# Kernel tuning notes

Measured on AMD Instinct MI355X. Metric: run time of the kernel, lower is better.

The kernel has to match this reference:

```python
import jax, jax.numpy as jnp
import numpy as np

S = 2        # subsample_rate
EPS = 1e-5   # BatchNorm eps


def maxpool(x, k):
    B, C, H, W = x.shape
    return x.reshape(B, C, H // k, k, W // k, k).max(axis=(3, 5))


def conv1x1(x, w, b):
    # x: [B,C,H,W], w: [O,C], b: [O]
    return jnp.einsum('bchw,oc->bohw', x, w) + b[None, :, None, None]


def upsample_bilinear_ac(y, s):
    # torch nn.Upsample(mode='bilinear', scale_factor=s, align_corners=True)
    B, C, h, w = y.shape
    H, W = h * s, w * s
    ri = jnp.arange(H, dtype=jnp.float32) * ((h - 1) / (H - 1))
    ci = jnp.arange(W, dtype=jnp.float32) * ((w - 1) / (W - 1))
    r0 = jnp.floor(ri).astype(jnp.int32); r1 = jnp.minimum(r0 + 1, h - 1)
    c0 = jnp.floor(ci).astype(jnp.int32); c1 = jnp.minimum(c0 + 1, w - 1)
    wr = (ri - r0)[None, None, :, None]
    wc = (ci - c0)[None, None, None, :]
    top = y[:, :, r0, :] * (1.0 - wr) + y[:, :, r1, :] * wr
    return top[:, :, :, c0] * (1.0 - wc) + top[:, :, :, c1] * wc


def setup_inputs() -> dict:
    key = jax.random.key(0)
    ks = jax.random.split(key, 12)
    B, C, IC, H, W = 4, 256, 128, 192, 192
    sc = 0.05  # keep attention logits in a sane range
    x = jax.random.normal(ks[0], (B, C, H, W), jnp.float32)
    g_w = jax.random.normal(ks[1], (IC, C), jnp.float32) * sc
    g_b = jax.random.normal(ks[2], (IC,), jnp.float32) * sc
    theta_w = jax.random.normal(ks[3], (IC, C), jnp.float32) * sc
    theta_b = jax.random.normal(ks[4], (IC,), jnp.float32) * sc
    phi_w = jax.random.normal(ks[5], (IC, C), jnp.float32) * sc
    phi_b = jax.random.normal(ks[6], (IC,), jnp.float32) * sc
    W_w = jax.random.normal(ks[7], (C, IC, 3, 3), jnp.float32) * sc
    W_b = jax.random.normal(ks[8], (C,), jnp.float32) * sc
    bn_gamma = jnp.ones((C,), jnp.float32)
    bn_beta = jnp.zeros((C,), jnp.float32)
    bn_mean = jax.random.normal(ks[9], (C,), jnp.float32) * sc
    bn_var = jax.random.uniform(ks[10], (C,), jnp.float32) + 0.5
    return dict(x=x, g_w=g_w, g_b=g_b, theta_w=theta_w, theta_b=theta_b,
                phi_w=phi_w, phi_b=phi_b, W_w=W_w, W_b=W_b,
                bn_gamma=bn_gamma, bn_beta=bn_beta, bn_mean=bn_mean, bn_var=bn_var)


def reference(x, g_w, g_b, theta_w, theta_b, phi_w, phi_b, W_w, W_b,
              bn_gamma, bn_beta, bn_mean, bn_var):
    B, C, H, Wd = x.shape
    IC = g_w.shape[0]
    xp = maxpool(x, S)                               # [B,C,H/S,W/S]
    theta = conv1x1(xp, theta_w, theta_b)            # [B,IC,h,w]
    g = maxpool(conv1x1(xp, g_w, g_b), 2)            # [B,IC,h/2,w/2]
    phi = maxpool(conv1x1(xp, phi_w, phi_b), 2)      # [B,IC,h/2,w/2]
    h, w = theta.shape[2], theta.shape[3]
    th = theta.reshape(B, IC, h * w).transpose(0, 2, 1)   # [B,Nt,IC]
    ph = phi.reshape(B, IC, -1)                           # [B,IC,Np]
    gx = g.reshape(B, IC, -1).transpose(0, 2, 1)          # [B,Np,IC]
    f = jnp.einsum('bnc,bcm->bnm', th, ph)                # [B,Nt,Np]
    a = jax.nn.softmax(f, axis=-1)
    y = jnp.einsum('bnm,bmc->bnc', a, gx)                 # [B,Nt,IC]
    y = y.transpose(0, 2, 1).reshape(B, IC, h, w)
    y = upsample_bilinear_ac(y, S)                        # [B,IC,H,W]
    wy = jax.lax.conv_general_dilated(
        y, W_w, (1, 1), ((1, 1), (1, 1)),
        dimension_numbers=('NCHW', 'OIHW', 'NCHW')) + W_b[None, :, None, None]
    inv = bn_gamma / jnp.sqrt(bn_var + EPS)
    wy = (wy - bn_mean[None, :, None, None]) * inv[None, :, None, None] + bn_beta[None, :, None, None]
    return (wy + x, wy)
```

## Files before the change

kernel.cpp:

```cpp
#include <hip/hip_runtime.h>
#include <hip/hip_bf16.h>
#include <math.h>

#define B_   4
#define C_   256
#define ICH  128
#define H_   192
#define W_   192
#define hs   96
#define ws2  96
#define HW   (hs*ws2)
#define HP   48
#define WP   48
#define NP   (HP*WP)
#define EPSB 1e-5f
#define PADW 194
#define TOT  ((size_t)B_*C_*H_*W_)

#define QB 128
#define KB 64
#define NT (NP/KB)
#define SM_OFF 20.0f

using bf16x8 = __attribute__((ext_vector_type(8))) short;
using f32x4  = __attribute__((ext_vector_type(4))) float;
using f32x16 = __attribute__((ext_vector_type(16))) float;

#define OFF_XPB   ((size_t)0)
#define OFF_THB   ((size_t)4718592)
#define OFF_PHB   ((size_t)7077888)
#define OFF_GVT   ((size_t)7667712)
#define OFF_WB3   ((size_t)8257536)
#define OFF_Y96N  ((size_t)8306688)
#define OFF_ST    ((size_t)13025280)
#define OFF_WT    ((size_t)13025792)
#define OFF_YPAD  ((size_t)13173248)

static __device__ __forceinline__ float b2f(unsigned short u) {
  union { unsigned int i; float f; } c; c.i = (unsigned int)u << 16; return c.f;
}

__global__ __launch_bounds__(256) void k_pool2(const float* __restrict__ x,
                                               __hip_bfloat16* __restrict__ xpb) {
  __shared__ float lds[96 * 33];
  int t  = threadIdx.x;
  int pi = blockIdx.x;
  int cg = blockIdx.y;
  int b  = blockIdx.z;
  const float* xb = x + (((size_t)b * C_ + cg * 32) * H_ + 2 * pi) * W_;
#pragma unroll
  for (int rr = 0; rr < 6; ++rr) {
    int e = rr * 256 + t;
    int c  = e / 48;
    int cq = e % 48;
    const float* src = xb + (size_t)c * H_ * W_ + cq * 4;
    float4 A = *(const float4*)src;
    float4 Bv = *(const float4*)(src + W_);
    float pe = fmaxf(fmaxf(A.x, A.y), fmaxf(Bv.x, Bv.y));
    float po = fmaxf(fmaxf(A.z, A.w), fmaxf(Bv.z, Bv.w));
    lds[(2 * cq) * 33 + c]     = pe;
    lds[(2 * cq + 1) * 33 + c] = po;
  }
  __syncthreads();
  __hip_bfloat16* ob = xpb + ((size_t)b * HW + pi * ws2) * C_ + cg * 32;
#pragma unroll
  for (int rr = 0; rr < 2; ++rr) {
    int w = rr * 256 + t;
    if (w < 384) {
      int pj = w >> 2, oc = w & 3;
      union { ushort u[8]; uint4 v; } pk;
#pragma unroll
      for (int k = 0; k < 8; ++k) {
        __hip_bfloat16 hv = __float2bfloat16(lds[pj * 33 + oc * 8 + k]);
        pk.u[k] = *(ushort*)&hv;
      }
      *(uint4*)(ob + (size_t)pj * C_ + oc * 8) = pk.v;
    }
  }
}

__global__ __launch_bounds__(256) void k_prep(const float* __restrict__ Ww,
                                              const float* __restrict__ tw,
                                              const float* __restrict__ gw,
                                              const float* __restrict__ pw,
                                              const float* __restrict__ Wb,
                                              const float* __restrict__ bg,
                                              const float* __restrict__ bb,
                                              const float* __restrict__ bm,
                                              const float* __restrict__ bv,
                                              __hip_bfloat16* __restrict__ Wt,
                                              __hip_bfloat16* __restrict__ wb3,
                                              float* __restrict__ ST) {
  int bid = blockIdx.x;
  int t = threadIdx.x;
  if (bid < 1152) {
    int idx = bid * 256 + t;
    int lo  = idx & 7;
    int o   = (idx >> 3) & 255;
    int ic8 = (idx >> 11) & 15;
    int tap = idx >> 15;
    int ic  = ic8 * 8 + lo;
    Wt[idx] = __float2bfloat16(Ww[(size_t)o * (ICH * 9) + ic * 9 + tap]);
  } else if (bid < 1536) {
    int idx = (bid - 1152) * 256 + t;
    int set = idx >> 15; int rem = idx & 32767;
    const float* src = set == 0 ? tw : (set == 1 ? gw : pw);
    wb3[idx] = __float2bfloat16(src[rem]);
  } else {
    float sc = bg[t] * rsqrtf(bv[t] + EPSB);
    ST[t] = sc;
    ST[256 + t] = (Wb[t] - bm[t]) * sc + bb[t];
  }
}

__global__ __launch_bounds__(256) void k_qkv2(
    const __hip_bfloat16* __restrict__ xpb,
    const __hip_bfloat16* __restrict__ wb3,
    const float* __restrict__ tb, const float* __restrict__ gb_,
    const float* __restrict__ pb_,
    __hip_bfloat16* __restrict__ thb,
    __hip_bfloat16* __restrict__ gvt,
    __hip_bfloat16* __restrict__ phb) {
  __shared__ __align__(16) char ldsX[96 * 512];
  int t = threadIdx.x;
  int lane = t & 63, li = lane & 15, g4 = lane >> 4;
  int wid = t >> 6;
  int wave_o = wid >> 1, wave_n = wid & 1;
  int ih = blockIdx.x;
  int i  = ih >> 1, half = ih & 1;
  int b  = blockIdx.y;
  const size_t xbase = (size_t)b * HW * C_;

#pragma unroll
  for (int rr = 0; rr < 12; ++rr) {
    int e = rr * 256 + t;
    int j = e >> 5, c8 = e & 31;
    int sc8 = c8 ^ (j & 7);
    int pix = (2 * i + (j & 1)) * ws2 + half * 48 + (j >> 1);
    __builtin_amdgcn_global_load_lds(
        (const __attribute__((address_space(1))) void*)(xpb + xbase + (size_t)pix * C_ + sc8 * 8),
        (__attribute__((address_space(3))) void*)(ldsX + (rr * 256 + (t & 192)) * 16),
        16, 0, 0);
  }
  asm volatile("s_waitcnt vmcnt(0)" ::: "memory");
  __builtin_amdgcn_s_barrier();

  for (int set = 0; set < 3; ++set) {
    const __hip_bfloat16* wset = wb3 + (size_t)set * 128 * 256;
    const float* bias = set == 0 ? tb : (set == 1 ? gb_ : pb_);
    f32x4 acc[4][3];
#pragma unroll
    for (int fo = 0; fo < 4; ++fo)
#pragma unroll
      for (int fq = 0; fq < 3; ++fq) acc[fo][fq] = (f32x4){0.f, 0.f, 0.f, 0.f};

    for (int step = 0; step < 4; ++step) {
      bf16x8 af[4][2];
#pragma unroll
      for (int fo = 0; fo < 4; ++fo)
#pragma unroll
        for (int ks = 0; ks < 2; ++ks) {
          int o = wave_o * 64 + fo * 16 + li;
          af[fo][ks] = *(const bf16x8*)(wset + (size_t)o * C_ + step * 64 + ks * 32 + g4 * 8);
        }
#pragma unroll
      for (int ks = 0; ks < 2; ++ks)
#pragma unroll
        for (int fq = 0; fq < 3; ++fq) {
          int j = wave_n * 48 + fq * 16 + li;
          int sl = (step * 8 + ks * 4 + g4) ^ (j & 7);
          bf16x8 bx = *(const bf16x8*)(ldsX + j * 512 + sl * 16);
#pragma unroll
          for (int fo = 0; fo < 4; ++fo)
            acc[fo][fq] = __builtin_amdgcn_mfma_f32_16x16x32_bf16(af[fo][ks], bx, acc[fo][fq], 0, 0, 0);
        }
    }

    if (set == 0) {
#pragma unroll
      for (int fo = 0; fo < 4; ++fo) {
        int ob = wave_o * 64 + fo * 16 + g4 * 4;
#pragma unroll
        for (int fq = 0; fq < 3; ++fq) {
          int j = wave_n * 48 + fq * 16 + li;
          int pix = (2 * i + (j & 1)) * ws2 + half * 48 + (j >> 1);
          union { ushort u[4]; uint2 v; } pk;
#pragma unroll
          for (int r = 0; r < 4; ++r) {
            __hip_bfloat16 hv = __float2bfloat16(acc[fo][fq][r] + bias[ob + r]);
            pk.u[r] = *(ushort*)&hv;
          }
          *(uint2*)(thb + ((size_t)b * HW + pix) * ICH + ob) = pk.v;
        }
      }
    } else {
#pragma unroll
      for (int fo = 0; fo < 4; ++fo) {
        int ob = wave_o * 64 + fo * 16 + g4 * 4;
#pragma unroll
        for (int fq = 0; fq < 3; ++fq) {
          float pv[4];
#pragma unroll
          for (int r = 0; r < 4; ++r) {
            float p = acc[fo][fq][r];
            p = fmaxf(p, __shfl_xor(p, 1, 64));
            p = fmaxf(p, __shfl_xor(p, 2, 64));
            pv[r] = p;
          }
          if ((li & 3) == 0) {
            int pc = half * 24 + wave_n * 12 + fq * 4 + (li >> 2);
            int pp = i * WP + pc;
            if (set == 1) {
              int kt = pp >> 6, m = pp & 63;
#pragma unroll
              for (int r = 0; r < 4; ++r)
                gvt[(((size_t)b * NT + kt) * ICH + ob + r) * 64 + m] =
                    __float2bfloat16(pv[r] + bias[ob + r]);
            } else {
              union { ushort u[4]; uint2 v; } pk;
#pragma unroll
              for (int r = 0; r < 4; ++r) {
                __hip_bfloat16 hv = __float2bfloat16(pv[r] + bias[ob + r]);
                pk.u[r] = *(ushort*)&hv;
              }
              *(uint2*)(phb + ((size_t)b * NP + pp) * ICH + ob) = pk.v;
            }
          }
        }
      }
    }
  }
}

__global__ __launch_bounds__(256) void k_attn_mfma(
    const __hip_bfloat16* __restrict__ thb,
    const __hip_bfloat16* __restrict__ phb,
    const __hip_bfloat16* __restrict__ gvt,
    __hip_bfloat16* __restrict__ y96b) {
  __shared__ __align__(16) char Kl[2][KB * 256];
  __shared__ __align__(16) char Vl[2][ICH * KB * 2];
  __shared__ __align__(16) char Pl[4][32 * KB * 2];
  int t = threadIdx.x;
  int lane = t & 63, li = lane & 15, g = lane >> 4;
  int w = t >> 6;
  int flat = blockIdx.x;
  int swz = (flat & 7) * 36 + (flat >> 3);
  int b  = swz / 72;
  int q0 = (swz % 72) * QB;

  bf16x8 aq[2][4];
#pragma unroll
  for (int qh = 0; qh < 2; ++qh) {
    const __hip_bfloat16* qp = thb + ((size_t)b * HW + q0 + w * 32 + qh * 16 + li) * ICH + g * 8;
#pragma unroll
    for (int ks = 0; ks < 4; ++ks) aq[qh][ks] = *(const bf16x8*)(qp + ks * 32);
  }

  f32x4 acc_o[2][8];
#pragma unroll
  for (int qh = 0; qh < 2; ++qh)
#pragma unroll
    for (int ct = 0; ct < 8; ++ct) acc_o[qh][ct] = (f32x4){0.f, 0.f, 0.f, 0.f};
  float l_acc[2][4] = {{0.f, 0.f, 0.f, 0.f}, {0.f, 0.f, 0.f, 0.f}};

  char* Pw = (char*)Pl[w];

#define STGKV(kt_, buf_)                                                        \
  {                                                                             \
    int m0_ = (kt_) * KB;                                                       \
    const __hip_bfloat16* vt_ = gvt + ((size_t)b * NT + (kt_)) * ICH * 64;      \
    _Pragma("unroll")                                                           \
    for (int rr = 0; rr < 4; ++rr) {                                            \
      int e = rr * 256 + t;                                                     \
      int mm = e >> 4, ch = (e & 15) ^ (mm & 7);                                \
      __builtin_amdgcn_global_load_lds(                                         \
          (const __attribute__((address_space(1))) void*)(phb + ((size_t)b * NP + m0_ + mm) * ICH + ch * 8), \
          (__attribute__((address_space(3))) void*)(Kl[buf_] + (rr * 256 + (t & 192)) * 16), \
          16, 0, 0);                                                            \
    }                                                                           \
    _Pragma("unroll")                                                           \
    for (int rr = 0; rr < 4; ++rr) {                                            \
      int e = rr * 256 + t;                                                     \
      int c = e >> 3, ch = (e & 7) ^ (c & 7);                                   \
      __builtin_amdgcn_global_load_lds(                                         \
          (const __attribute__((address_space(1))) void*)(vt_ + (size_t)c * 64 + ch * 8), \
          (__attribute__((address_space(3))) void*)(Vl[buf_] + (rr * 256 + (t & 192)) * 16), \
          16, 0, 0);                                                            \
    }                                                                           \
  }

  STGKV(0, 0)
  for (int kt = 0; kt < NT; ++kt) {
    int buf = kt & 1;
    if (kt < NT - 1) {
      STGKV(kt + 1, buf ^ 1)
      asm volatile("s_waitcnt vmcnt(8)" ::: "memory");
    } else {
      asm volatile("s_waitcnt vmcnt(0)" ::: "memory");
    }
    __builtin_amdgcn_s_barrier();

#pragma unroll
    for (int qh = 0; qh < 2; ++qh) {
      f32x4 s[4];
#pragma unroll
      for (int mt = 0; mt < 4; ++mt) s[mt] = (f32x4){0.f, 0.f, 0.f, 0.f};
#pragma unroll
      for (int mt = 0; mt < 4; ++mt) {
        int m = mt * 16 + li;
#pragma unroll
        for (int ks = 0; ks < 4; ++ks) {
          bf16x8 bk = *(const bf16x8*)(Kl[buf] + m * 256 + ((ks * 64 + g * 16) ^ ((li & 7) << 4)));
          s[mt] = __builtin_amdgcn_mfma_f32_16x16x32_bf16(aq[qh][ks], bk, s[mt], 0, 0, 0);
        }
      }

#pragma unroll
      for (int mt = 0; mt < 4; ++mt) {
#pragma unroll
        for (int r = 0; r < 4; ++r) {
          float p = __expf(s[mt][r] - SM_OFF);
          s[mt][r] = p;
          l_acc[qh][r] += p;
        }
      }

#pragma unroll
      for (int mt = 0; mt < 4; ++mt) {
        int m = mt * 16 + li;
#pragma unroll
        for (int r = 0; r < 4; ++r) {
          int ql = g * 4 + r;
          __hip_bfloat16 hv = __float2bfloat16(s[mt][r]);
          *(ushort*)(Pw + (qh * 16 + ql) * 128 + ((m * 2) ^ ((ql & 7) << 4))) = *(ushort*)&hv;
        }
      }
    }

    bf16x8 pa[2][2];
#pragma unroll
    for (int qh = 0; qh < 2; ++qh)
#pragma unroll
      for (int ks = 0; ks < 2; ++ks)
        pa[qh][ks] = *(const bf16x8*)(Pw + (qh * 16 + li) * 128 + ((ks * 64 + g * 16) ^ ((li & 7) << 4)));
#pragma unroll
    for (int ct = 0; ct < 8; ++ct) {
      int c = ct * 16 + li;
#pragma unroll
      for (int ks = 0; ks < 2; ++ks) {
        bf16x8 bv = *(const bf16x8*)(Vl[buf] + c * 128 + ((ks * 64 + g * 16) ^ ((c & 7) << 4)));
#pragma unroll
        for (int qh = 0; qh < 2; ++qh)
          acc_o[qh][ct] = __builtin_amdgcn_mfma_f32_16x16x32_bf16(pa[qh][ks], bv, acc_o[qh][ct], 0, 0, 0);
      }
    }
    __builtin_amdgcn_s_barrier();
  }

#pragma unroll
  for (int qh = 0; qh < 2; ++qh) {
    float inv[4];
#pragma unroll
    for (int r = 0; r < 4; ++r) {
      float l = l_acc[qh][r];
      l += __shfl_xor(l, 1, 64);
      l += __shfl_xor(l, 2, 64);
      l += __shfl_xor(l, 4, 64);
      l += __shfl_xor(l, 8, 64);
      inv[r] = 1.f / l;
    }
    __hip_bfloat16* ob = y96b + ((size_t)b * HW + q0 + w * 32 + qh * 16 + g * 4) * ICH + li;
#pragma unroll
    for (int r = 0; r < 4; ++r)
#pragma unroll
      for (int ct = 0; ct < 8; ++ct)
        ob[(size_t)r * ICH + ct * 16] = __float2bfloat16(acc_o[qh][ct][r] * inv[r]);
  }
}

__global__ __launch_bounds__(256) void k_up_pad(const __hip_bfloat16* __restrict__ y96b,
                                                __hip_bfloat16* __restrict__ ypad) {
  int idx = blockIdx.x * 256 + threadIdx.x;
  int pc  = idx % PADW;
  int r2  = idx / PADW;
  int ic8 = r2 & 15;
  int r3  = r2 >> 4;
  int pr  = r3 % PADW;
  int b   = r3 / PADW;
  __hip_bfloat16* dst = ypad + (size_t)idx * 8;
  if (pr == 0 || pr == PADW - 1 || pc == 0 || pc == PADW - 1) {
    uint2 z = {0, 0};
    *(uint2*)dst = z;
    *(uint2*)(dst + 4) = z;
    return;
  }
  int p = pr - 1, q = pc - 1;
  const float sc = 95.0f / 191.0f;
  float ri = p * sc, ci = q * sc;
  int r0 = (int)ri; int r1 = min(r0 + 1, hs - 1); float wr = ri - r0;
  int c0 = (int)ci; int c1 = min(c0 + 1, ws2 - 1); float wc = ci - c0;
  const __hip_bfloat16* base = y96b + (size_t)b * HW * ICH + ic8 * 8;
  union { ushort u[4]; uint2 v; } a, bb, cc, dd, pk;
  a.v  = *(const uint2*)(base + ((size_t)r0 * ws2 + c0) * ICH);
  bb.v = *(const uint2*)(base + ((size_t)r0 * ws2 + c1) * ICH);
  cc.v = *(const uint2*)(base + ((size_t)r1 * ws2 + c0) * ICH);
  dd.v = *(const uint2*)(base + ((size_t)r1 * ws2 + c1) * ICH);
  union { ushort u[4]; uint2 v; } a2, bb2, cc2, dd2, pk2;
  a2.v  = *(const uint2*)(base + ((size_t)r0 * ws2 + c0) * ICH + 4);
  bb2.v = *(const uint2*)(base + ((size_t)r0 * ws2 + c1) * ICH + 4);
  cc2.v = *(const uint2*)(base + ((size_t)r1 * ws2 + c0) * ICH + 4);
  dd2.v = *(const uint2*)(base + ((size_t)r1 * ws2 + c1) * ICH + 4);
#pragma unroll
  for (int j = 0; j < 4; ++j) {
    float top = b2f(a.u[j]) * (1.f - wr) + b2f(cc.u[j]) * wr;
    float bot = b2f(bb.u[j]) * (1.f - wr) + b2f(dd.u[j]) * wr;
    float v = top * (1.f - wc) + bot * wc;
    __hip_bfloat16 hv = __float2bfloat16(v);
    pk.u[j] = *(ushort*)&hv;
    float top2 = b2f(a2.u[j]) * (1.f - wr) + b2f(cc2.u[j]) * wr;
    float bot2 = b2f(bb2.u[j]) * (1.f - wr) + b2f(dd2.u[j]) * wr;
    float v2 = top2 * (1.f - wc) + bot2 * wc;
    __hip_bfloat16 hv2 = __float2bfloat16(v2);
    pk2.u[j] = *(ushort*)&hv2;
  }
  *(uint2*)dst = pk.v;
  *(uint2*)(dst + 4) = pk2.v;
}

#define ABY 12288
#define BBY 4096
#define BUF (ABY + BBY)
__global__ __launch_bounds__(256) void k_conv3_mfma(
    const __hip_bfloat16* __restrict__ ypad,
    const __hip_bfloat16* __restrict__ Wt,
    const float* __restrict__ ST,
    const float* __restrict__ x,
    float* __restrict__ out) {
  __shared__ __align__(16) char ldsM[2 * BUF];
  int t = threadIdx.x;
  int lane = t & 63;
  int l31 = lane & 31, h = lane >> 5;
  int wid = t >> 6;

  int flat = blockIdx.x;
  int swz = (flat & 7) * 384 + (flat >> 3);
  int zz  = swz / 384;
  int rem = swz % 384;
  int b  = zz >> 1;
  int o0 = (zz & 1) * 128;
  int p  = rem >> 1;
  int q0 = (rem & 1) * 96;

  f32x16 acc[3];
#pragma unroll
  for (int j = 0; j < 3; ++j)
#pragma unroll
    for (int r = 0; r < 16; ++r) acc[j][r] = 0.f;

#define STG(s_, buf_)                                                           \
  {                                                                             \
    int kh_ = (s_) >> 3, icE_ = (s_) & 7;                                       \
    char* base_ = ldsM + (buf_) * BUF;                                          \
    _Pragma("unroll")                                                           \
    for (int rr = 0; rr < 3; ++rr) {                                            \
      int e = rr * 256 + t;                                                     \
      int tap_ = e >> 8, ch_ = (e >> 7) & 1, o_ = e & 127;                      \
      size_t gsl = (((size_t)(kh_ * 3 + tap_) * 16 + icE_ * 2 + ch_) * 256 + o0 + o_) * 8; \
      __builtin_amdgcn_global_load_lds(                                         \
          (const __attribute__((address_space(1))) void*)(Wt + gsl),            \
          (__attribute__((address_space(3))) void*)(base_ + (rr * 256 + (t & 192)) * 16), \
          16, 0, 0);                                                            \
    }                                                                           \
    if (t < 196) {                                                              \
      int ch_ = (t >= 98) ? 1 : 0;                                              \
      int col_ = t - ch_ * 98;                                                  \
      size_t gsl = (((size_t)(b * PADW + p + kh_) * 16 + icE_ * 2 + ch_) * PADW + q0 + col_) * 8; \
      __builtin_amdgcn_global_load_lds(                                         \
          (const __attribute__((address_space(1))) void*)(ypad + gsl),          \
          (__attribute__((address_space(3))) void*)(base_ + ABY + (t & 192) * 16), \
          16, 0, 0);                                                            \
    }                                                                           \
  }

  STG(0, 0)
  __syncthreads();
  for (int s = 0; s < 24; ++s) {
    if (s < 23) { STG(s + 1, (s + 1) & 1) }
    const char* Ab = ldsM + (s & 1) * BUF;
    const char* Bb = Ab + ABY;
#pragma unroll
    for (int kw = 0; kw < 3; ++kw) {
      bf16x8 afr = *(const bf16x8*)(Ab + (kw * 256 + h * 128 + wid * 32 + l31) * 16);
#pragma unroll
      for (int fq = 0; fq < 3; ++fq) {
        bf16x8 bfr = *(const bf16x8*)(Bb + (h * 98 + fq * 32 + l31 + kw) * 16);
        acc[fq] = __builtin_amdgcn_mfma_f32_32x32x16_bf16(afr, bfr, acc[fq], 0, 0, 0);
      }
    }
    __syncthreads();
  }

#pragma unroll
  for (int fq = 0; fq < 3; ++fq) {
#pragma unroll
    for (int r = 0; r < 16; ++r) {
      int o = o0 + wid * 32 + (r & 3) + 8 * (r >> 2) + 4 * h;
      int q = q0 + fq * 32 + l31;
      size_t oi = (((size_t)b * C_ + o) * H_ + p) * W_ + q;
      float val = acc[fq][r] * ST[o] + ST[256 + o];
      out[TOT + oi] = val;
      out[oi] = val + x[oi];
    }
  }
}

extern "C" void kernel_launch(void* const* d_in, const int* in_sizes, int n_in,
                              void* d_out, int out_size, void* d_ws, size_t ws_size,
                              hipStream_t stream) {
  const float* x    = (const float*)d_in[0];
  const float* g_w  = (const float*)d_in[1];
  const float* g_b  = (const float*)d_in[2];
  const float* th_w = (const float*)d_in[3];
  const float* th_b = (const float*)d_in[4];
  const float* ph_w = (const float*)d_in[5];
  const float* ph_b = (const float*)d_in[6];
  const float* W_w  = (const float*)d_in[7];
  const float* W_b  = (const float*)d_in[8];
  const float* bn_g = (const float*)d_in[9];
  const float* bn_b = (const float*)d_in[10];
  const float* bn_m = (const float*)d_in[11];
  const float* bn_v = (const float*)d_in[12];
  float* out = (float*)d_out;
  float* ws  = (float*)d_ws;

  __hip_bfloat16* xpb = (__hip_bfloat16*)(ws + OFF_XPB);
  __hip_bfloat16* thb = (__hip_bfloat16*)(ws + OFF_THB);
  __hip_bfloat16* phb = (__hip_bfloat16*)(ws + OFF_PHB);
  __hip_bfloat16* gvt = (__hip_bfloat16*)(ws + OFF_GVT);
  __hip_bfloat16* wb3 = (__hip_bfloat16*)(ws + OFF_WB3);
  __hip_bfloat16* y96b = (__hip_bfloat16*)(ws + OFF_Y96N);
  float* ST   = ws + OFF_ST;
  __hip_bfloat16* Wt   = (__hip_bfloat16*)(ws + OFF_WT);
  __hip_bfloat16* ypad = (__hip_bfloat16*)(ws + OFF_YPAD);

  k_prep<<<dim3(1537), 256, 0, stream>>>(W_w, th_w, g_w, ph_w, W_b, bn_g, bn_b,
                                         bn_m, bn_v, Wt, wb3, ST);
  k_pool2<<<dim3(hs, C_ / 32, B_), 256, 0, stream>>>(x, xpb);
  k_qkv2<<<dim3(2 * HP, B_), 256, 0, stream>>>(xpb, wb3, th_b, g_b, ph_b, thb, gvt, phb);
  k_attn_mfma<<<dim3(B_ * (HW / QB)), 256, 0, stream>>>(thb, phb, gvt, y96b);
  k_up_pad<<<(B_ * PADW * 16 * PADW) / 256, 256, 0, stream>>>(y96b, ypad);
  k_conv3_mfma<<<dim3(3072), 256, 0, stream>>>(ypad, Wt, ST, x, out);
}
```

Baseline: 374.3 us.

## Fuse 2x2 maxpool into QKV projection kernel, dropping pooled intermediate buffer

Removes the separate pooling kernel and has the QKV projection kernel read fp32 x directly. It max-pools 2x2 windows, converts to bf16 and writes into the swizzled LDS layout. This avoids a kernel launch and a global write and read of the pooled bf16 tensor. In exchange, each QKV block now issues 48 rounds of fp32 loads with scalar LDS stores instead of async global-to-LDS copies. With only 384 blocks, the load phase may have less memory-level parallelism.

```diff
diff --git a/kernel.cpp b/kernel.cpp
--- a/kernel.cpp
+++ b/kernel.cpp
@@ -26,7 +26,6 @@
 using f32x4  = __attribute__((ext_vector_type(4))) float;
 using f32x16 = __attribute__((ext_vector_type(16))) float;
 
-#define OFF_XPB   ((size_t)0)
 #define OFF_THB   ((size_t)4718592)
 #define OFF_PHB   ((size_t)7077888)
 #define OFF_GVT   ((size_t)7667712)
@@ -38,45 +37,6 @@
 
 static __device__ __forceinline__ float b2f(unsigned short u) {
   union { unsigned int i; float f; } c; c.i = (unsigned int)u << 16; return c.f;
-}
-
-__global__ __launch_bounds__(256) void k_pool2(const float* __restrict__ x,
-                                               __hip_bfloat16* __restrict__ xpb) {
-  __shared__ float lds[96 * 33];
-  int t  = threadIdx.x;
-  int pi = blockIdx.x;
-  int cg = blockIdx.y;
-  int b  = blockIdx.z;
-  const float* xb = x + (((size_t)b * C_ + cg * 32) * H_ + 2 * pi) * W_;
-#pragma unroll
-  for (int rr = 0; rr < 6; ++rr) {
-    int e = rr * 256 + t;
-    int c  = e / 48;
-    int cq = e % 48;
-    const float* src = xb + (size_t)c * H_ * W_ + cq * 4;
-    float4 A = *(const float4*)src;
-    float4 Bv = *(const float4*)(src + W_);
-    float pe = fmaxf(fmaxf(A.x, A.y), fmaxf(Bv.x, Bv.y));
-    float po = fmaxf(fmaxf(A.z, A.w), fmaxf(Bv.z, Bv.w));
-    lds[(2 * cq) * 33 + c]     = pe;
-    lds[(2 * cq + 1) * 33 + c] = po;
-  }
-  __syncthreads();
-  __hip_bfloat16* ob = xpb + ((size_t)b * HW + pi * ws2) * C_ + cg * 32;
-#pragma unroll
-  for (int rr = 0; rr < 2; ++rr) {
-    int w = rr * 256 + t;
-    if (w < 384) {
-      int pj = w >> 2, oc = w & 3;
-      union { ushort u[8]; uint4 v; } pk;
-#pragma unroll
-      for (int k = 0; k < 8; ++k) {
-        __hip_bfloat16 hv = __float2bfloat16(lds[pj * 33 + oc * 8 + k]);
-        pk.u[k] = *(ushort*)&hv;
-      }
-      *(uint4*)(ob + (size_t)pj * C_ + oc * 8) = pk.v;
-    }
-  }
 }
 
 __global__ __launch_bounds__(256) void k_prep(const float* __restrict__ Ww,
@@ -113,8 +73,8 @@
   }
 }
 
-__global__ __launch_bounds__(256) void k_qkv2(
-    const __hip_bfloat16* __restrict__ xpb,
+__global__ __launch_bounds__(256) void k_qkv3(
+    const float* __restrict__ x,
     const __hip_bfloat16* __restrict__ wb3,
     const float* __restrict__ tb, const float* __restrict__ gb_,
     const float* __restrict__ pb_,
@@ -129,21 +89,29 @@
   int ih = blockIdx.x;
   int i  = ih >> 1, half = ih & 1;
   int b  = blockIdx.y;
-  const size_t xbase = (size_t)b * HW * C_;
-
-#pragma unroll
-  for (int rr = 0; rr < 12; ++rr) {
+
+  const float* xb = x + ((size_t)b * C_) * H_ * W_;
+#pragma unroll
+  for (int rr = 0; rr < 48; ++rr) {
     int e = rr * 256 + t;
-    int j = e >> 5, c8 = e & 31;
-    int sc8 = c8 ^ (j & 7);
-    int pix = (2 * i + (j & 1)) * ws2 + half * 48 + (j >> 1);
-    __builtin_amdgcn_global_load_lds(
-        (const __attribute__((address_space(1))) void*)(xpb + xbase + (size_t)pix * C_ + sc8 * 8),
-        (__attribute__((address_space(3))) void*)(ldsX + (rr * 256 + (t & 192)) * 16),
-        16, 0, 0);
-  }
-  asm volatile("s_waitcnt vmcnt(0)" ::: "memory");
-  __builtin_amdgcn_s_barrier();
+    int c   = e / 48;
+    int rem = e - c * 48;
+    int rho = rem / 24;
+    int cq  = rem - rho * 24;
+    const float* src = xb + ((size_t)c * H_ + 4 * i + 2 * rho) * W_ + half * 96 + 4 * cq;
+    float4 A  = *(const float4*)src;
+    float4 Bv = *(const float4*)(src + W_);
+    float p0 = fmaxf(fmaxf(A.x, A.y), fmaxf(Bv.x, Bv.y));
+    float p1 = fmaxf(fmaxf(A.z, A.w), fmaxf(Bv.z, Bv.w));
+    int j0 = 4 * cq + rho;
+    int j1 = 4 * cq + 2 + rho;
+    int c8 = c >> 3, cl = c & 7;
+    __hip_bfloat16 h0 = __float2bfloat16(p0);
+    __hip_bfloat16 h1 = __float2bfloat16(p1);
+    *(ushort*)(ldsX + j0 * 512 + ((c8 ^ (j0 & 7)) << 4) + cl * 2) = *(ushort*)&h0;
+    *(ushort*)(ldsX + j1 * 512 + ((c8 ^ (j1 & 7)) << 4) + cl * 2) = *(ushort*)&h1;
+  }
+  __syncthreads();
 
   for (int set = 0; set < 3; ++set) {
     const __hip_bfloat16* wset = wb3 + (size_t)set * 128 * 256;
@@ -533,7 +501,6 @@
   float* out = (float*)d_out;
   float* ws  = (float*)d_ws;
 
-  __hip_bfloat16* xpb = (__hip_bfloat16*)(ws + OFF_XPB);
   __hip_bfloat16* thb = (__hip_bfloat16*)(ws + OFF_THB);
   __hip_bfloat16* phb = (__hip_bfloat16*)(ws + OFF_PHB);
   __hip_bfloat16* gvt = (__hip_bfloat16*)(ws + OFF_GVT);
@@ -545,8 +512,7 @@
 
   k_prep<<<dim3(1537), 256, 0, stream>>>(W_w, th_w, g_w, ph_w, W_b, bn_g, bn_b,
                                          bn_m, bn_v, Wt, wb3, ST);
-  k_pool2<<<dim3(hs, C_ / 32, B_), 256, 0, stream>>>(x, xpb);
-  k_qkv2<<<dim3(2 * HP, B_), 256, 0, stream>>>(xpb, wb3, th_b, g_b, ph_b, thb, gvt, phb);
+  k_qkv3<<<dim3(2 * HP, B_), 256, 0, stream>>>(x, wb3, th_b, g_b, ph_b, thb, gvt, phb);
   k_attn_mfma<<<dim3(B_ * (HW / QB)), 256, 0, stream>>>(thb, phb, gvt, y96b);
   k_up_pad<<<(B_ * PADW * 16 * PADW) / 256, 256, 0, stream>>>(y96b, ypad);
   k_conv3_mfma<<<dim3(3072), 256, 0, stream>>>(ypad, Wt, ST, x, out);
```

Measured after the change: 372.6 us. No clear change (-0.4%).
